# Performance work log

Hardware: AMD Instinct MI355X
Metric: run time of the kernel (lower is better)

## Reference

```python
import jax, jax.numpy as jnp
import numpy as np

N_NODES = 100000
N_EDGES = 3200000
IN_DIM = 256
HID_DIM = 64
OUT_DIM = 64


def setup_inputs() -> dict:
    key = jax.random.key(0)
    k1, k2, k3, k4, k5, k6 = jax.random.split(key, 6)
    x = jax.random.normal(k1, (N_NODES, IN_DIM), dtype=jnp.float32)
    edge_index = jax.random.randint(k2, (2, N_EDGES), 0, N_NODES, dtype=jnp.int32)
    # Glorot-style init for the two GCNConv layers (PyG default: glorot weight, zero bias)
    W1 = jax.random.normal(k3, (IN_DIM, HID_DIM), dtype=jnp.float32) * (1.0 / np.sqrt(IN_DIM))
    b1 = jnp.zeros((HID_DIM,), dtype=jnp.float32)
    W2 = jax.random.normal(k4, (HID_DIM, OUT_DIM), dtype=jnp.float32) * (1.0 / np.sqrt(HID_DIM))
    b2 = jnp.zeros((OUT_DIM,), dtype=jnp.float32)
    return {"x": x, "edge_index": edge_index, "W1": W1, "b1": b1, "W2": W2, "b2": b2}


def _gcn_conv(x, src, dst, deg_inv_sqrt, W, b, n):
    # PyG GCNConv: h = x W; out_i = sum_j norm_ij * h_j + b, with symmetric norm
    h = x @ W                                   # (n, d_out) small GEMM
    norm = deg_inv_sqrt[src] * deg_inv_sqrt[dst]  # (E+n,)
    msg = norm[:, None] * h[src]                # gather (E+n, d_out)
    agg = jax.ops.segment_sum(msg, dst, num_segments=n)  # scatter-add
    return agg + b


def reference(x, edge_index, W1, b1, W2, b2):
    n = x.shape[0]
    loops = jnp.arange(n, dtype=edge_index.dtype)
    src = jnp.concatenate([edge_index[0], loops])
    dst = jnp.concatenate([edge_index[1], loops])
    # degree on destination (col) with added self-loops, weight 1.0
    deg = jax.ops.segment_sum(jnp.ones_like(dst, dtype=x.dtype), dst, num_segments=n)
    deg_inv_sqrt = jnp.where(deg > 0, jax.lax.rsqrt(deg), 0.0)
    h = jax.nn.relu(_gcn_conv(x, src, dst, deg_inv_sqrt, W1, b1, n))
    return _gcn_conv(h, src, dst, deg_inv_sqrt, W2, b2, n)
```

## Files before the change

### kernel.cpp

```cpp
#include <hip/hip_runtime.h>
#include <cstdint>
#include <cstddef>


#define BIN_SHIFT 7
#define BIN_NODES 128
#define MAX_BINS 1024
#define SUP_SHIFT 11
#define FINE_PER_SUP 16
#define NSUP_MAX 64
#define SCAP 56
#define SRC_BITS 17
#define SRC_MASK ((1 << SRC_BITS) - 1)

typedef unsigned short ushort_t;

typedef __attribute__((ext_vector_type(8))) short bf16x8;
typedef __attribute__((ext_vector_type(4))) float f32x4;

union FragB {
  uint4 u;
  bf16x8 b;
};

__device__ __forceinline__ float4 bfq2f4(uint2 p) {
  float4 r;
  r.x = __uint_as_float(p.x << 16);
  r.y = __uint_as_float(p.x & 0xFFFF0000u);
  r.z = __uint_as_float(p.y << 16);
  r.w = __uint_as_float(p.y & 0xFFFF0000u);
  return r;
}
__device__ __forceinline__ unsigned f2bf(float f) {
  unsigned u = __float_as_uint(f);
  return (u + 0x7FFFu + ((u >> 16) & 1u)) >> 16;
}
__device__ __forceinline__ uint2 f42bfq(float4 f) {
  uint2 r;
  r.x = f2bf(f.x) | (f2bf(f.y) << 16);
  r.y = f2bf(f.z) | (f2bf(f.w) << 16);
  return r;
}

__global__ void zero_int(int* __restrict__ p, int n) {
  int i = blockIdx.x * blockDim.x + threadIdx.x;
  if (i < n) p[i] = 0;
}

__global__ __launch_bounds__(256) void bin_count(const int* __restrict__ dst, int E, int nbins,
                                                 int* __restrict__ binCnt) {
  __shared__ int h[MAX_BINS];
  for (int i = threadIdx.x; i < nbins; i += 256) h[i] = 0;
  __syncthreads();
  int stride = gridDim.x * 256;
  for (int e = blockIdx.x * 256 + threadIdx.x; e < E; e += stride)
    atomicAdd(&h[dst[e] >> BIN_SHIFT], 1);
  __syncthreads();
  for (int i = threadIdx.x; i < nbins; i += 256)
    if (h[i]) atomicAdd(&binCnt[i], h[i]);
}

__global__ __launch_bounds__(256) void bin_scan(const int* __restrict__ binCnt, int nbins, int E,
                                                int* __restrict__ binStart,
                                                int* __restrict__ binCursor,
                                                int* __restrict__ supCursor) {
  __shared__ int s[256];
  int t = threadIdx.x;
  int c[4];
  int sum = 0;
#pragma unroll
  for (int i = 0; i < 4; i++) {
    int idx = t * 4 + i;
    c[i] = (idx < nbins) ? binCnt[idx] : 0;
    sum += c[i];
  }
  int v = sum;
  s[t] = v;
  __syncthreads();
  for (int d = 1; d < 256; d <<= 1) {
    int add = (t >= d) ? s[t - d] : 0;
    __syncthreads();
    s[t] += add;
    __syncthreads();
  }
  int run = s[t] - v;
#pragma unroll
  for (int i = 0; i < 4; i++) {
    int idx = t * 4 + i;
    if (idx < nbins) {
      binStart[idx] = run;
      binCursor[idx] = run;
      if ((idx & (FINE_PER_SUP - 1)) == 0) supCursor[idx >> 4] = run;
      run += c[i];
    }
  }
  if (t == 0) binStart[nbins] = E;
}

__global__ __launch_bounds__(256) void super_fill(const int* __restrict__ src,
                                                  const int* __restrict__ dst, int E, int nsup,
                                                  int* __restrict__ supCursor,
                                                  unsigned* __restrict__ supbuf) {
  __shared__ unsigned stage[NSUP_MAX * SCAP];
  __shared__ int lcnt[NSUP_MAX], lbase[NSUP_MAX], lscan[NSUP_MAX + 1];
  int chunk = (E + gridDim.x - 1) / gridDim.x;
  int c0 = blockIdx.x * chunk;
  int c1 = min(E, c0 + chunk);
  for (int t0 = c0; t0 < c1; t0 += 2048) {
    int t1 = min(c1, t0 + 2048);
    if (threadIdx.x < nsup) lcnt[threadIdx.x] = 0;
    __syncthreads();
    for (int e = t0 + threadIdx.x; e < t1; e += 256) {
      int d = dst[e];
      int sb = d >> SUP_SHIFT;
      unsigned v = ((unsigned)(d & ((1 << SUP_SHIFT) - 1)) << SRC_BITS) | (unsigned)src[e];
      int idx = atomicAdd(&lcnt[sb], 1);
      if (idx < SCAP)
        stage[sb * SCAP + idx] = v;
      else {
        int g = atomicAdd(&supCursor[sb], 1);
        supbuf[g] = v;
      }
    }
    __syncthreads();
    if (threadIdx.x < nsup) {
      int c = min(lcnt[threadIdx.x], SCAP);
      lcnt[threadIdx.x] = c;
      lbase[threadIdx.x] = c ? atomicAdd(&supCursor[threadIdx.x], c) : 0;
    }
    __syncthreads();
    if (threadIdx.x == 0) {
      int r = 0;
      for (int i = 0; i < nsup; i++) {
        lscan[i] = r;
        r += lcnt[i];
      }
      lscan[nsup] = r;
    }
    __syncthreads();
    int total = lscan[nsup];
    for (int j = threadIdx.x; j < total; j += 256) {
      int lo = 0, hi = nsup;
      while (hi - lo > 1) {
        int mid = (lo + hi) >> 1;
        if (lscan[mid] <= j)
          lo = mid;
        else
          hi = mid;
      }
      int off = j - lscan[lo];
      supbuf[lbase[lo] + off] = stage[lo * SCAP + off];
    }
    __syncthreads();
  }
}

__global__ __launch_bounds__(256) void fine_fill(const unsigned* __restrict__ supbuf,
                                                 const int* __restrict__ binStart, int nbins,
                                                 int* __restrict__ binCursor,
                                                 unsigned* __restrict__ binbuf) {
  __shared__ int lcnt[FINE_PER_SUP], lbase[FINE_PER_SUP];
  int sb = blockIdx.x >> 3, p = blockIdx.x & 7;
  int seg0 = binStart[sb << 4];
  int seg1 = binStart[min((sb + 1) << 4, nbins)];
  int part = (seg1 - seg0 + 7) >> 3;
  int c0 = seg0 + p * part;
  int c1 = min(seg1, c0 + part);
  if (threadIdx.x < FINE_PER_SUP) lcnt[threadIdx.x] = 0;
  __syncthreads();
  for (int i = c0 + threadIdx.x; i < c1; i += 256) atomicAdd(&lcnt[supbuf[i] >> 24], 1);
  __syncthreads();
  if (threadIdx.x < FINE_PER_SUP) {
    int c = lcnt[threadIdx.x];
    lbase[threadIdx.x] = c ? atomicAdd(&binCursor[(sb << 4) + threadIdx.x], c) : 0;
    lcnt[threadIdx.x] = 0;
  }
  __syncthreads();
  for (int i = c0 + threadIdx.x; i < c1; i += 256) {
    unsigned v = supbuf[i];
    unsigned dls = v >> SRC_BITS;
    int f = dls >> BIN_SHIFT;
    unsigned vf = ((dls & (BIN_NODES - 1)) << SRC_BITS) | (v & SRC_MASK);
    int idx = lbase[f] + atomicAdd(&lcnt[f], 1);
    binbuf[idx] = vf;
  }
}

__global__ __launch_bounds__(256) void node_count_dis(const unsigned* __restrict__ binbuf,
                                                      const int* __restrict__ binStart, int N,
                                                      int* __restrict__ count,
                                                      float* __restrict__ dis) {
  __shared__ int cnt[BIN_NODES];
  int b = blockIdx.x;
  int nodeBase = b << BIN_SHIFT;
  if (threadIdx.x < BIN_NODES) cnt[threadIdx.x] = 0;
  __syncthreads();
  int s0 = binStart[b], s1 = binStart[b + 1];
  for (int i = s0 + threadIdx.x; i < s1; i += 256) atomicAdd(&cnt[binbuf[i] >> SRC_BITS], 1);
  __syncthreads();
  if (threadIdx.x < BIN_NODES) {
    int node = nodeBase + threadIdx.x;
    if (node < N) {
      int c = cnt[threadIdx.x];
      count[node] = c;
      dis[node] = rsqrtf((float)(c + 1));
    }
  }
}

__global__ __launch_bounds__(256) void bin_csr(const unsigned* __restrict__ binbuf,
                                               const int* __restrict__ binStart,
                                               const int* __restrict__ count, int N, int E,
                                               int* __restrict__ rowptr, int* __restrict__ col) {
  __shared__ int cur[BIN_NODES];
  __shared__ int pref[BIN_NODES];
  int b = blockIdx.x, t = threadIdx.x;
  int nodeBase = b << BIN_SHIFT;
  int c = 0;
  if (t < BIN_NODES) {
    int node = nodeBase + t;
    c = (node < N) ? count[node] : 0;
    pref[t] = c;
  }
  __syncthreads();
  for (int d = 1; d < BIN_NODES; d <<= 1) {
    int add = (t < BIN_NODES && t >= d) ? pref[t - d] : 0;
    __syncthreads();
    if (t < BIN_NODES) pref[t] += add;
    __syncthreads();
  }
  int s0 = binStart[b];
  if (t < BIN_NODES) {
    int node = nodeBase + t;
    if (node < N) {
      int ex = s0 + pref[t] - c;
      rowptr[node] = ex;
      cur[t] = ex;
    }
  }
  if (b == 0 && t == 255) rowptr[N] = E;
  __syncthreads();
  int s1 = binStart[b + 1];
  for (int i = s0 + t; i < s1; i += 256) {
    unsigned v = binbuf[i];
    int slot = atomicAdd(&cur[v >> SRC_BITS], 1);
    col[slot] = v & SRC_MASK;
  }
}

__global__ __launch_bounds__(256) void wsplit(const float* __restrict__ W1,
                                              const float* __restrict__ W2,
                                              ushort_t* __restrict__ wt1,
                                              ushort_t* __restrict__ wt2) {
  int i = blockIdx.x * 256 + threadIdx.x;
  const float* W;
  ushort_t* wt;
  int K, idx;
  if (i < 256 * 64) {
    W = W1; wt = wt1; K = 256; idx = i;
  } else if (i < 256 * 64 + 64 * 64) {
    W = W2; wt = wt2; K = 64; idx = i - 256 * 64;
  } else
    return;
  int n = idx & 63, k = idx >> 6;
  float f = W[k * 64 + n];
  unsigned u = __float_as_uint(f);
  unsigned hb = u & 0xFFFF0000u;
  float lo = f - __uint_as_float(hb);
  wt[(size_t)n * K + k] = (ushort_t)(u >> 16);
  wt[(size_t)64 * K + (size_t)n * K + k] = (ushort_t)(__float_as_uint(lo) >> 16);
}

__device__ __forceinline__ void split8u(uint4 a, uint4 b, uint4& xh, uint4& xl) {
  unsigned ua[8] = {a.x, a.y, a.z, a.w, b.x, b.y, b.z, b.w};
  unsigned hw[4], lw[4];
#pragma unroll
  for (int p = 0; p < 4; p++) {
    unsigned u0 = ua[2 * p], u1 = ua[2 * p + 1];
    unsigned h0 = u0 & 0xFFFF0000u, h1 = u1 & 0xFFFF0000u;
    float l0 = __uint_as_float(u0) - __uint_as_float(h0);
    float l1 = __uint_as_float(u1) - __uint_as_float(h1);
    hw[p] = (u0 >> 16) | h1;
    lw[p] = (__float_as_uint(l0) >> 16) | (__float_as_uint(l1) & 0xFFFF0000u);
  }
  xh = make_uint4(hw[0], hw[1], hw[2], hw[3]);
  xl = make_uint4(lw[0], lw[1], lw[2], lw[3]);
}

template <int K, bool ABF16>
__global__ __launch_bounds__(256, 3) void gemm_mfma(const void* __restrict__ Av,
                                                    const ushort_t* __restrict__ Wt,
                                                    uint2* __restrict__ Cb, int M) {
  const int lane = threadIdx.x & 63;
  const int wv = threadIdx.x >> 6;
  const int l15 = lane & 15;
  const int lq = lane >> 4;
  const int m0 = blockIdx.x * 128 + wv * 32;

  const ushort_t* __restrict__ Wlo = Wt + (size_t)64 * K;

  f32x4 acc[2][4];
#pragma unroll
  for (int a = 0; a < 2; a++)
#pragma unroll
    for (int b = 0; b < 4; b++) acc[a][b] = (f32x4){0.f, 0.f, 0.f, 0.f};

  int node[2], ncl[2];
#pragma unroll
  for (int mt = 0; mt < 2; mt++) {
    node[mt] = m0 + mt * 16 + l15;
    ncl[mt] = node[mt] < M ? node[mt] : (M - 1);
  }

  if (ABF16) {
    constexpr int NT = K / 32;
    FragB xa[NT][2], wh[NT][4], wl[NT][4];
#pragma unroll
    for (int t = 0; t < NT; t++)
#pragma unroll
      for (int mt = 0; mt < 2; mt++)
        xa[t][mt].u = *(const uint4*)((const ushort_t*)Av + (size_t)ncl[mt] * K + t * 32 + lq * 8);
#pragma unroll
    for (int t = 0; t < NT; t++)
#pragma unroll
      for (int nt = 0; nt < 4; nt++) {
        wh[t][nt].u = *(const uint4*)(Wt + (size_t)(nt * 16 + l15) * K + t * 32 + lq * 8);
        wl[t][nt].u = *(const uint4*)(Wlo + (size_t)(nt * 16 + l15) * K + t * 32 + lq * 8);
      }
#pragma unroll
    for (int t = 0; t < NT; t++)
#pragma unroll
      for (int mt = 0; mt < 2; mt++)
#pragma unroll
        for (int nt = 0; nt < 4; nt++) {
          acc[mt][nt] =
              __builtin_amdgcn_mfma_f32_16x16x32_bf16(wh[t][nt].b, xa[t][mt].b, acc[mt][nt], 0, 0, 0);
          acc[mt][nt] =
              __builtin_amdgcn_mfma_f32_16x16x32_bf16(wl[t][nt].b, xa[t][mt].b, acc[mt][nt], 0, 0, 0);
        }
  } else {
    constexpr int NT = K / 32;
    const float* __restrict__ A = (const float*)Av;
    uint4 xp[2][2][2];
    FragB wh[2][4];
    FragB wlc[4];

#pragma unroll
    for (int nt = 0; nt < 4; nt++)
      wh[0][nt].u = *(const uint4*)(Wt + (size_t)(nt * 16 + l15) * K + lq * 8);
#pragma unroll
    for (int t = 0; t < 2; t++)
#pragma unroll
      for (int mt = 0; mt < 2; mt++) {
        const float* p = A + (size_t)ncl[mt] * K + t * 32 + lq * 8;
        xp[t][mt][0] = *(const uint4*)p;
        xp[t][mt][1] = *(const uint4*)(p + 4);
      }

#pragma unroll
    for (int kt = 0; kt < NT; kt++) {
      const int cs = kt & 1;
      const int kb = kt * 32 + lq * 8;
      if (kt + 1 < NT) {
        const int kbn = (kt + 1) * 32 + lq * 8;
#pragma unroll
        for (int nt = 0; nt < 4; nt++)
          wh[cs ^ 1][nt].u = *(const uint4*)(Wt + (size_t)(nt * 16 + l15) * K + kbn);
      }
#pragma unroll
      for (int nt = 0; nt < 4; nt++)
        wlc[nt].u = *(const uint4*)(Wlo + (size_t)(nt * 16 + l15) * K + kb);
      uint4 c0a = xp[cs][0][0], c0b = xp[cs][0][1];
      uint4 c1a = xp[cs][1][0], c1b = xp[cs][1][1];
      if (kt + 2 < NT) {
#pragma unroll
        for (int mt = 0; mt < 2; mt++) {
          const float* p = A + (size_t)ncl[mt] * K + (kt + 2) * 32 + lq * 8;
          xp[cs][mt][0] = *(const uint4*)p;
          xp[cs][mt][1] = *(const uint4*)(p + 4);
        }
      }
      FragB xh0, xl0, xh1, xl1;
      split8u(c0a, c0b, xh0.u, xl0.u);
      split8u(c1a, c1b, xh1.u, xl1.u);
#pragma unroll
      for (int nt = 0; nt < 4; nt++) {
        acc[0][nt] = __builtin_amdgcn_mfma_f32_16x16x32_bf16(wh[cs][nt].b, xh0.b, acc[0][nt], 0, 0, 0);
        acc[0][nt] = __builtin_amdgcn_mfma_f32_16x16x32_bf16(wh[cs][nt].b, xl0.b, acc[0][nt], 0, 0, 0);
        acc[1][nt] = __builtin_amdgcn_mfma_f32_16x16x32_bf16(wh[cs][nt].b, xh1.b, acc[1][nt], 0, 0, 0);
        acc[1][nt] = __builtin_amdgcn_mfma_f32_16x16x32_bf16(wh[cs][nt].b, xl1.b, acc[1][nt], 0, 0, 0);
      }
#pragma unroll
      for (int nt = 0; nt < 4; nt++) {
        acc[0][nt] = __builtin_amdgcn_mfma_f32_16x16x32_bf16(wlc[nt].b, xh0.b, acc[0][nt], 0, 0, 0);
        acc[1][nt] = __builtin_amdgcn_mfma_f32_16x16x32_bf16(wlc[nt].b, xh1.b, acc[1][nt], 0, 0, 0);
      }
    }
  }

#pragma unroll
  for (int mt = 0; mt < 2; mt++) {
    if (node[mt] < M) {
      uint2* cp = Cb + (size_t)node[mt] * 16 + lq;
#pragma unroll
      for (int nt = 0; nt < 4; nt++) {
        float4 o = make_float4(acc[mt][nt][0], acc[mt][nt][1], acc[mt][nt][2], acc[mt][nt][3]);
        cp[nt * 4] = f42bfq(o);
      }
    }
  }
}

template <bool OUTBF>
__global__ __launch_bounds__(256) void agg_kernel(
    const uint2* __restrict__ h, const int* __restrict__ rowptr, const int* __restrict__ col,
    const float* __restrict__ dis, const float* __restrict__ bias, void* __restrict__ outv,
    int N, int relu) {
  int wid = (blockIdx.x * blockDim.x + threadIdx.x) >> 6;
  if (wid >= N) return;
  int lane = threadIdx.x & 63;
  int sub = lane & 15;
  int quarter = lane >> 4;

  int start = rowptr[wid], end = rowptr[wid + 1];
  float di = dis[wid];

  float4 a0 = make_float4(0.f, 0.f, 0.f, 0.f), a1 = a0, a2 = a0, a3 = a0;
  {
    float4 self = bfq2f4(h[(size_t)wid * 16 + sub]);
    if (quarter == 0) {
      a0.x = di * self.x;
      a0.y = di * self.y;
      a0.z = di * self.z;
      a0.w = di * self.w;
    }
  }

  for (int base = start; base < end; base += 64) {
    int e = base + lane;
    int sj = 0;
    float wj = 0.f;
    if (e < end) {
      sj = col[e];
      wj = dis[sj];
    }
    int cnt = end - base;
    if (cnt > 64) cnt = 64;
    int rounds = (cnt + 3) >> 2;
    int t = 0;
    for (; t + 4 <= rounds; t += 4) {
      int i0 = 4 * t + quarter;
      int s0 = __shfl(sj, i0), s1 = __shfl(sj, i0 + 4), s2 = __shfl(sj, i0 + 8),
          s3 = __shfl(sj, i0 + 12);
      float w0 = __shfl(wj, i0), w1 = __shfl(wj, i0 + 4), w2 = __shfl(wj, i0 + 8),
            w3 = __shfl(wj, i0 + 12);
      float4 g0 = bfq2f4(h[(size_t)s0 * 16 + sub]);
      float4 g1 = bfq2f4(h[(size_t)s1 * 16 + sub]);
      float4 g2 = bfq2f4(h[(size_t)s2 * 16 + sub]);
      float4 g3 = bfq2f4(h[(size_t)s3 * 16 + sub]);
      a0.x += w0 * g0.x; a0.y += w0 * g0.y; a0.z += w0 * g0.z; a0.w += w0 * g0.w;
      a1.x += w1 * g1.x; a1.y += w1 * g1.y; a1.z += w1 * g1.z; a1.w += w1 * g1.w;
      a2.x += w2 * g2.x; a2.y += w2 * g2.y; a2.z += w2 * g2.z; a2.w += w2 * g2.w;
      a3.x += w3 * g3.x; a3.y += w3 * g3.y; a3.z += w3 * g3.z; a3.w += w3 * g3.w;
    }
    for (; t < rounds; t++) {
      int i0 = 4 * t + quarter;
      int s0 = __shfl(sj, i0);
      float w0 = __shfl(wj, i0);
      float4 g0 = bfq2f4(h[(size_t)s0 * 16 + sub]);
      a0.x += w0 * g0.x; a0.y += w0 * g0.y; a0.z += w0 * g0.z; a0.w += w0 * g0.w;
    }
  }

  float sx = (a0.x + a1.x) + (a2.x + a3.x);
  float sy = (a0.y + a1.y) + (a2.y + a3.y);
  float sz = (a0.z + a1.z) + (a2.z + a3.z);
  float sw = (a0.w + a1.w) + (a2.w + a3.w);
  sx += __shfl_down(sx, 32); sy += __shfl_down(sy, 32);
  sz += __shfl_down(sz, 32); sw += __shfl_down(sw, 32);
  sx += __shfl_down(sx, 16); sy += __shfl_down(sy, 16);
  sz += __shfl_down(sz, 16); sw += __shfl_down(sw, 16);
  if (quarter == 0) {
    float4 bv = ((const float4*)bias)[sub];
    float4 o = make_float4(di * sx + bv.x, di * sy + bv.y, di * sz + bv.z, di * sw + bv.w);
    if (relu) {
      o.x = fmaxf(o.x, 0.f);
      o.y = fmaxf(o.y, 0.f);
      o.z = fmaxf(o.z, 0.f);
      o.w = fmaxf(o.w, 0.f);
    }
    if (OUTBF)
      ((uint2*)outv)[(size_t)wid * 16 + sub] = f42bfq(o);
    else
      ((float4*)outv)[(size_t)wid * 16 + sub] = o;
  }
}

extern "C" void kernel_launch(void* const* d_in, const int* in_sizes, int n_in,
                              void* d_out, int out_size, void* d_ws, size_t ws_size,
                              hipStream_t stream) {
  const float* x = (const float*)d_in[0];
  const int* ei = (const int*)d_in[1];
  const float* W1 = (const float*)d_in[2];
  const float* b1 = (const float*)d_in[3];
  const float* W2 = (const float*)d_in[4];
  const float* b2 = (const float*)d_in[5];

  const int IN = 256;
  const int E = in_sizes[1] / 2;
  const int N = in_sizes[0] / IN;
  const int* src = ei;
  const int* dst = ei + E;
  const int nbins = (N + BIN_NODES - 1) >> BIN_SHIFT;
  const int nsup = (N + (1 << SUP_SHIFT) - 1) >> SUP_SHIFT;

  char* ws = (char*)d_ws;
  size_t off = 0;
  auto alloc = [&](size_t bytes) -> void* {
    void* p = ws + off;
    off += (bytes + 255) & ~(size_t)255;
    return p;
  };
  int* count = (int*)alloc((size_t)N * 4);
  int* rowptr = (int*)alloc((size_t)(N + 1) * 4);
  float* dis = (float*)alloc((size_t)N * 4);
  int* binCnt = (int*)alloc(MAX_BINS * 4);
  int* binStart = (int*)alloc((MAX_BINS + 1) * 4);
  int* binCursor = (int*)alloc(MAX_BINS * 4);
  int* supCursor = (int*)alloc(NSUP_MAX * 4);
  int* col = (int*)alloc((size_t)E * 4);
  unsigned* supbuf = (unsigned*)col;
  uint2* out1 = (uint2*)alloc((size_t)N * 64 * 2);
  size_t big = ((size_t)E * 4 > (size_t)N * 128) ? (size_t)E * 4 : (size_t)N * 128;
  unsigned* binbuf = (unsigned*)alloc(big);
  uint2* h = (uint2*)binbuf;
  ushort_t* wt1 = (ushort_t*)alloc((size_t)2 * 64 * 256 * 2);
  ushort_t* wt2 = (ushort_t*)alloc((size_t)2 * 64 * 64 * 2);
  float* outf = (float*)d_out;

  zero_int<<<(nbins + 255) / 256, 256, 0, stream>>>(binCnt, nbins);
  bin_count<<<1024, 256, 0, stream>>>(dst, E, nbins, binCnt);
  bin_scan<<<1, 256, 0, stream>>>(binCnt, nbins, E, binStart, binCursor, supCursor);
  super_fill<<<512, 256, 0, stream>>>(src, dst, E, nsup, supCursor, supbuf);
  fine_fill<<<nsup * 8, 256, 0, stream>>>(supbuf, binStart, nbins, binCursor, binbuf);
  node_count_dis<<<nbins, 256, 0, stream>>>(binbuf, binStart, N, count, dis);
  bin_csr<<<nbins, 256, 0, stream>>>(binbuf, binStart, count, N, E, rowptr, col);
  wsplit<<<(256 * 64 + 64 * 64 + 255) / 256, 256, 0, stream>>>(W1, W2, wt1, wt2);

  gemm_mfma<256, false><<<(N + 127) / 128, 256, 0, stream>>>(x, wt1, h, N);
  agg_kernel<true><<<(N + 3) / 4, 256, 0, stream>>>(h, rowptr, col, dis, b1, out1, N, 1);
  gemm_mfma<64, true><<<(N + 127) / 128, 256, 0, stream>>>(out1, wt2, h, N);
  agg_kernel<false><<<(N + 3) / 4, 256, 0, stream>>>(h, rowptr, col, dis, b2, outf, N, 0);
}
```

Baseline: 473.9 us.

## Stage GEMM1 input via async global-to-LDS loads and one-tile super_fill blocks

The first GEMM now streams x tiles into swizzled LDS with global_load_lds, keeping a triple buffer and manual vmcnt waits to overlap loads with MFMA work. Weight fragments are double-buffered in registers. super_fill now launches one block per 2048-edge tile, preloads src/dst into registers and replaces the serial lane-0 scan with a wave shuffle scan. This adds LDS use and hand-tuned wait counts that must match the issued load count, which could hurt occupancy or correctness.

```diff
diff --git a/kernel.cpp b/kernel.cpp
--- a/kernel.cpp
+++ b/kernel.cpp
@@ -103,17 +103,28 @@
                                                   unsigned* __restrict__ supbuf) {
   __shared__ unsigned stage[NSUP_MAX * SCAP];
   __shared__ int lcnt[NSUP_MAX], lbase[NSUP_MAX], lscan[NSUP_MAX + 1];
-  int chunk = (E + gridDim.x - 1) / gridDim.x;
-  int c0 = blockIdx.x * chunk;
-  int c1 = min(E, c0 + chunk);
-  for (int t0 = c0; t0 < c1; t0 += 2048) {
-    int t1 = min(c1, t0 + 2048);
-    if (threadIdx.x < nsup) lcnt[threadIdx.x] = 0;
-    __syncthreads();
-    for (int e = t0 + threadIdx.x; e < t1; e += 256) {
-      int d = dst[e];
+  const int tid = threadIdx.x;
+  const int t0 = blockIdx.x * 2048;
+  const int t1 = min(E, t0 + 2048);
+
+  int dv[8], sv[8];
+#pragma unroll
+  for (int i = 0; i < 8; i++) {
+    int e = t0 + i * 256 + tid;
+    if (e < t1) {
+      dv[i] = dst[e];
+      sv[i] = src[e];
+    }
+  }
+  if (tid < nsup) lcnt[tid] = 0;
+  __syncthreads();
+#pragma unroll
+  for (int i = 0; i < 8; i++) {
+    int e = t0 + i * 256 + tid;
+    if (e < t1) {
+      int d = dv[i];
       int sb = d >> SUP_SHIFT;
-      unsigned v = ((unsigned)(d & ((1 << SUP_SHIFT) - 1)) << SRC_BITS) | (unsigned)src[e];
+      unsigned v = ((unsigned)(d & ((1 << SUP_SHIFT) - 1)) << SRC_BITS) | (unsigned)sv[i];
       int idx = atomicAdd(&lcnt[sb], 1);
       if (idx < SCAP)
         stage[sb * SCAP + idx] = v;
@@ -122,36 +133,38 @@
         supbuf[g] = v;
       }
     }
-    __syncthreads();
-    if (threadIdx.x < nsup) {
-      int c = min(lcnt[threadIdx.x], SCAP);
-      lcnt[threadIdx.x] = c;
-      lbase[threadIdx.x] = c ? atomicAdd(&supCursor[threadIdx.x], c) : 0;
-    }
-    __syncthreads();
-    if (threadIdx.x == 0) {
-      int r = 0;
-      for (int i = 0; i < nsup; i++) {
-        lscan[i] = r;
-        r += lcnt[i];
-      }
-      lscan[nsup] = r;
-    }
-    __syncthreads();
-    int total = lscan[nsup];
-    for (int j = threadIdx.x; j < total; j += 256) {
-      int lo = 0, hi = nsup;
-      while (hi - lo > 1) {
-        int mid = (lo + hi) >> 1;
-        if (lscan[mid] <= j)
-          lo = mid;
-        else
-          hi = mid;
-      }
-      int off = j - lscan[lo];
-      supbuf[lbase[lo] + off] = stage[lo * SCAP + off];
-    }
-    __syncthreads();
+  }
+  __syncthreads();
+  if (tid < nsup) {
+    int c = min(lcnt[tid], SCAP);
+    lcnt[tid] = c;
+    lbase[tid] = c ? atomicAdd(&supCursor[tid], c) : 0;
+  }
+  __syncthreads();
+  if (tid < 64) {
+    int vv = (tid < nsup) ? lcnt[tid] : 0;
+    int ss = vv;
+#pragma unroll
+    for (int d = 1; d < 64; d <<= 1) {
+      int u = __shfl_up(ss, d);
+      if (tid >= d) ss += u;
+    }
+    lscan[tid + 1] = ss;
+    if (tid == 0) lscan[0] = 0;
+  }
+  __syncthreads();
+  int total = lscan[nsup];
+  for (int j = tid; j < total; j += 256) {
+    int lo = 0, hi = nsup;
+    while (hi - lo > 1) {
+      int mid = (lo + hi) >> 1;
+      if (lscan[mid] <= j)
+        lo = mid;
+      else
+        hi = mid;
+    }
+    int off = j - lscan[lo];
+    supbuf[lbase[lo] + off] = stage[lo * SCAP + off];
   }
 }
 
@@ -287,10 +300,11 @@
   xl = make_uint4(lw[0], lw[1], lw[2], lw[3]);
 }
 
-template <int K, bool ABF16>
-__global__ __launch_bounds__(256, 3) void gemm_mfma(const void* __restrict__ Av,
-                                                    const ushort_t* __restrict__ Wt,
-                                                    uint2* __restrict__ Cb, int M) {
+__global__ __launch_bounds__(256, 3) void gemm1_mfma(const float* __restrict__ A,
+                                                     const ushort_t* __restrict__ Wt,
+                                                     uint2* __restrict__ Cb, int M) {
+  constexpr int K = 256;
+  __shared__ uint4 xtile[3][4][256];
   const int lane = threadIdx.x & 63;
   const int wv = threadIdx.x >> 6;
   const int l15 = lane & 15;
@@ -305,6 +319,108 @@
 #pragma unroll
     for (int b = 0; b < 4; b++) acc[a][b] = (f32x4){0.f, 0.f, 0.f, 0.f};
 
+  auto stage_tile = [&](int kt, int buf) {
+#pragma unroll
+    for (int c = 0; c < 4; c++) {
+      int s = c * 64 + lane;
+      int r = s >> 3;
+      int c4 = (s & 7) ^ (r & 7);
+      int nd = m0 + r;
+      if (nd >= M) nd = M - 1;
+      const float* gp = A + (size_t)nd * K + kt * 32 + c4 * 4;
+      __builtin_amdgcn_global_load_lds(
+          (const __attribute__((address_space(1))) void*)gp,
+          (__attribute__((address_space(3))) void*)&xtile[buf][wv][c * 64], 16, 0, 0);
+    }
+  };
+  auto load_w = [&](int kt, FragB* wr) {
+    const int kb = kt * 32 + lq * 8;
+#pragma unroll
+    for (int nt = 0; nt < 4; nt++) {
+      wr[nt].u = *(const uint4*)(Wt + (size_t)(nt * 16 + l15) * K + kb);
+      wr[4 + nt].u = *(const uint4*)(Wlo + (size_t)(nt * 16 + l15) * K + kb);
+    }
+  };
+
+  FragB w[2][8];
+  stage_tile(0, 0);
+  load_w(0, w[0]);
+  __builtin_amdgcn_sched_barrier(0);
+  stage_tile(1, 1);
+  __builtin_amdgcn_sched_barrier(0);
+
+#pragma unroll
+  for (int j = 0; j < 8; j++) {
+    if (j < 7)
+      asm volatile("s_waitcnt vmcnt(12)" ::: "memory");
+    else
+      asm volatile("s_waitcnt vmcnt(8)" ::: "memory");
+    __builtin_amdgcn_sched_barrier(0);
+    uint4 xa[2][2];
+#pragma unroll
+    for (int mt = 0; mt < 2; mt++) {
+      int mr = mt * 16 + l15;
+#pragma unroll
+      for (int hh = 0; hh < 2; hh++) {
+        int c4 = (lq * 2 + hh) ^ (mr & 7);
+        xa[mt][hh] = *(const uint4*)&xtile[j % 3][wv][mr * 8 + c4];
+      }
+    }
+    if (j + 1 < 8) load_w(j + 1, w[(j + 1) & 1]);
+    __builtin_amdgcn_sched_barrier(0);
+    if (j + 2 < 8) stage_tile(j + 2, (j + 2) % 3);
+    __builtin_amdgcn_sched_barrier(0);
+    FragB xh0, xl0, xh1, xl1;
+    split8u(xa[0][0], xa[0][1], xh0.u, xl0.u);
+    split8u(xa[1][0], xa[1][1], xh1.u, xl1.u);
+    const FragB* wc = w[j & 1];
+#pragma unroll
+    for (int nt = 0; nt < 4; nt++) {
+      acc[0][nt] = __builtin_amdgcn_mfma_f32_16x16x32_bf16(wc[nt].b, xh0.b, acc[0][nt], 0, 0, 0);
+      acc[0][nt] = __builtin_amdgcn_mfma_f32_16x16x32_bf16(wc[nt].b, xl0.b, acc[0][nt], 0, 0, 0);
+      acc[1][nt] = __builtin_amdgcn_mfma_f32_16x16x32_bf16(wc[nt].b, xh1.b, acc[1][nt], 0, 0, 0);
+      acc[1][nt] = __builtin_amdgcn_mfma_f32_16x16x32_bf16(wc[nt].b, xl1.b, acc[1][nt], 0, 0, 0);
+    }
+#pragma unroll
+    for (int nt = 0; nt < 4; nt++) {
+      acc[0][nt] = __builtin_amdgcn_mfma_f32_16x16x32_bf16(wc[4 + nt].b, xh0.b, acc[0][nt], 0, 0, 0);
+      acc[1][nt] = __builtin_amdgcn_mfma_f32_16x16x32_bf16(wc[4 + nt].b, xh1.b, acc[1][nt], 0, 0, 0);
+    }
+  }
+
+#pragma unroll
+  for (int mt = 0; mt < 2; mt++) {
+    int node = m0 + mt * 16 + l15;
+    if (node < M) {
+      uint2* cp = Cb + (size_t)node * 16 + lq;
+#pragma unroll
+      for (int nt = 0; nt < 4; nt++) {
+        float4 o = make_float4(acc[mt][nt][0], acc[mt][nt][1], acc[mt][nt][2], acc[mt][nt][3]);
+        cp[nt * 4] = f42bfq(o);
+      }
+    }
+  }
+}
+
+__global__ __launch_bounds__(256, 3) void gemm2_mfma(const ushort_t* __restrict__ Av,
+                                                     const ushort_t* __restrict__ Wt,
+                                                     uint2* __restrict__ Cb, int M) {
+  constexpr int K = 64;
+  constexpr int NT = K / 32;
+  const int lane = threadIdx.x & 63;
+  const int wv = threadIdx.x >> 6;
+  const int l15 = lane & 15;
+  const int lq = lane >> 4;
+  const int m0 = blockIdx.x * 128 + wv * 32;
+
+  const ushort_t* __restrict__ Wlo = Wt + (size_t)64 * K;
+
+  f32x4 acc[2][4];
+#pragma unroll
+  for (int a = 0; a < 2; a++)
+#pragma unroll
+    for (int b = 0; b < 4; b++) acc[a][b] = (f32x4){0.f, 0.f, 0.f, 0.f};
+
   int node[2], ncl[2];
 #pragma unroll
   for (int mt = 0; mt < 2; mt++) {
@@ -312,91 +428,30 @@
     ncl[mt] = node[mt] < M ? node[mt] : (M - 1);
   }
 
-  if (ABF16) {
-    constexpr int NT = K / 32;
-    FragB xa[NT][2], wh[NT][4], wl[NT][4];
-#pragma unroll
-    for (int t = 0; t < NT; t++)
-#pragma unroll
-      for (int mt = 0; mt < 2; mt++)
-        xa[t][mt].u = *(const uint4*)((const ushort_t*)Av + (size_t)ncl[mt] * K + t * 32 + lq * 8);
-#pragma unroll
-    for (int t = 0; t < NT; t++)
+  FragB xa[NT][2], wh[NT][4], wl[NT][4];
+#pragma unroll
+  for (int t = 0; t < NT; t++)
+#pragma unroll
+    for (int mt = 0; mt < 2; mt++)
+      xa[t][mt].u = *(const uint4*)(Av + (size_t)ncl[mt] * K + t * 32 + lq * 8);
+#pragma unroll
+  for (int t = 0; t < NT; t++)
+#pragma unroll
+    for (int nt = 0; nt < 4; nt++) {
+      wh[t][nt].u = *(const uint4*)(Wt + (size_t)(nt * 16 + l15) * K + t * 32 + lq * 8);
+      wl[t][nt].u = *(const uint4*)(Wlo + (size_t)(nt * 16 + l15) * K + t * 32 + lq * 8);
+    }
+#pragma unroll
+  for (int t = 0; t < NT; t++)
+#pragma unroll
+    for (int mt = 0; mt < 2; mt++)
 #pragma unroll
       for (int nt = 0; nt < 4; nt++) {
-        wh[t][nt].u = *(const uint4*)(Wt + (size_t)(nt * 16 + l15) * K + t * 32 + lq * 8);
-        wl[t][nt].u = *(const uint4*)(Wlo + (size_t)(nt * 16 + l15) * K + t * 32 + lq * 8);
+        acc[mt][nt] =
+            __builtin_amdgcn_mfma_f32_16x16x32_bf16(wh[t][nt].b, xa[t][mt].b, acc[mt][nt], 0, 0, 0);
+        acc[mt][nt] =
+            __builtin_amdgcn_mfma_f32_16x16x32_bf16(wl[t][nt].b, xa[t][mt].b, acc[mt][nt], 0, 0, 0);
       }
-#pragma unroll
-    for (int t = 0; t < NT; t++)
-#pragma unroll
-      for (int mt = 0; mt < 2; mt++)
-#pragma unroll
-        for (int nt = 0; nt < 4; nt++) {
-          acc[mt][nt] =
-              __builtin_amdgcn_mfma_f32_16x16x32_bf16(wh[t][nt].b, xa[t][mt].b, acc[mt][nt], 0, 0, 0);
-          acc[mt][nt] =
-              __builtin_amdgcn_mfma_f32_16x16x32_bf16(wl[t][nt].b, xa[t][mt].b, acc[mt][nt], 0, 0, 0);
-        }
-  } else {
-    constexpr int NT = K / 32;
-    const float* __restrict__ A = (const float*)Av;
-    uint4 xp[2][2][2];
-    FragB wh[2][4];
-    FragB wlc[4];
-
-#pragma unroll
-    for (int nt = 0; nt < 4; nt++)
-      wh[0][nt].u = *(const uint4*)(Wt + (size_t)(nt * 16 + l15) * K + lq * 8);
-#pragma unroll
-    for (int t = 0; t < 2; t++)
-#pragma unroll
-      for (int mt = 0; mt < 2; mt++) {
-        const float* p = A + (size_t)ncl[mt] * K + t * 32 + lq * 8;
-        xp[t][mt][0] = *(const uint4*)p;
-        xp[t][mt][1] = *(const uint4*)(p + 4);
-      }
-
-#pragma unroll
-    for (int kt = 0; kt < NT; kt++) {
-      const int cs = kt & 1;
-      const int kb = kt * 32 + lq * 8;
-      if (kt + 1 < NT) {
-        const int kbn = (kt + 1) * 32 + lq * 8;
-#pragma unroll
-        for (int nt = 0; nt < 4; nt++)
-          wh[cs ^ 1][nt].u = *(const uint4*)(Wt + (size_t)(nt * 16 + l15) * K + kbn);
-      }
-#pragma unroll
-      for (int nt = 0; nt < 4; nt++)
-        wlc[nt].u = *(const uint4*)(Wlo + (size_t)(nt * 16 + l15) * K + kb);
-      uint4 c0a = xp[cs][0][0], c0b = xp[cs][0][1];
-      uint4 c1a = xp[cs][1][0], c1b = xp[cs][1][1];
-      if (kt + 2 < NT) {
-#pragma unroll
-        for (int mt = 0; mt < 2; mt++) {
-          const float* p = A + (size_t)ncl[mt] * K + (kt + 2) * 32 + lq * 8;
-          xp[cs][mt][0] = *(const uint4*)p;
-          xp[cs][mt][1] = *(const uint4*)(p + 4);
-        }
-      }
-      FragB xh0, xl0, xh1, xl1;
-      split8u(c0a, c0b, xh0.u, xl0.u);
-      split8u(c1a, c1b, xh1.u, xl1.u);
-#pragma unroll
-      for (int nt = 0; nt < 4; nt++) {
-        acc[0][nt] = __builtin_amdgcn_mfma_f32_16x16x32_bf16(wh[cs][nt].b, xh0.b, acc[0][nt], 0, 0, 0);
-        acc[0][nt] = __builtin_amdgcn_mfma_f32_16x16x32_bf16(wh[cs][nt].b, xl0.b, acc[0][nt], 0, 0, 0);
-        acc[1][nt] = __builtin_amdgcn_mfma_f32_16x16x32_bf16(wh[cs][nt].b, xh1.b, acc[1][nt], 0, 0, 0);
-        acc[1][nt] = __builtin_amdgcn_mfma_f32_16x16x32_bf16(wh[cs][nt].b, xl1.b, acc[1][nt], 0, 0, 0);
-      }
-#pragma unroll
-      for (int nt = 0; nt < 4; nt++) {
-        acc[0][nt] = __builtin_amdgcn_mfma_f32_16x16x32_bf16(wlc[nt].b, xh0.b, acc[0][nt], 0, 0, 0);
-        acc[1][nt] = __builtin_amdgcn_mfma_f32_16x16x32_bf16(wlc[nt].b, xh1.b, acc[1][nt], 0, 0, 0);
-      }
-    }
-  }
 
 #pragma unroll
   for (int mt = 0; mt < 2; mt++) {
@@ -541,14 +596,14 @@
   zero_int<<<(nbins + 255) / 256, 256, 0, stream>>>(binCnt, nbins);
   bin_count<<<1024, 256, 0, stream>>>(dst, E, nbins, binCnt);
   bin_scan<<<1, 256, 0, stream>>>(binCnt, nbins, E, binStart, binCursor, supCursor);
-  super_fill<<<512, 256, 0, stream>>>(src, dst, E, nsup, supCursor, supbuf);
+  super_fill<<<(E + 2047) / 2048, 256, 0, stream>>>(src, dst, E, nsup, supCursor, supbuf);
   fine_fill<<<nsup * 8, 256, 0, stream>>>(supbuf, binStart, nbins, binCursor, binbuf);
   node_count_dis<<<nbins, 256, 0, stream>>>(binbuf, binStart, N, count, dis);
   bin_csr<<<nbins, 256, 0, stream>>>(binbuf, binStart, count, N, E, rowptr, col);
   wsplit<<<(256 * 64 + 64 * 64 + 255) / 256, 256, 0, stream>>>(W1, W2, wt1, wt2);
 
-  gemm_mfma<256, false><<<(N + 127) / 128, 256, 0, stream>>>(x, wt1, h, N);
+  gemm1_mfma<<<(N + 127) / 128, 256, 0, stream>>>(x, wt1, h, N);
   agg_kernel<true><<<(N + 3) / 4, 256, 0, stream>>>(h, rowptr, col, dis, b1, out1, N, 1);
-  gemm_mfma<64, true><<<(N + 127) / 128, 256, 0, stream>>>(out1, wt2, h, N);
+  gemm2_mfma<<<(N + 127) / 128, 256, 0, stream>>>((const ushort_t*)out1, wt2, h, N);
   agg_kernel<false><<<(N + 3) / 4, 256, 0, stream>>>(h, rowptr, col, dis, b2, outf, N, 0);
 }
```

Result: faster. 463.6 us (-2.2%).
